# Performance work log

Measured on AMD Instinct MI355X. Metric: run time of the kernel, lower is better.

## Reference

```python
import jax, jax.numpy as jnp
import numpy as np

N_NODES = 100000
N_EDGES = 3200000
IN_DIM = 128
HID = 64


def _gcn_conv(x, src, dst, norm, W, b, n_nodes):
    # x: [N, Fin]; PyG GCNConv: h = x @ W^T, propagate with sym norm, + bias
    h = x @ W.T                                  # [N, Fout]
    msg = h[src] * norm[:, None]                 # gather + scale, [E', Fout]
    out = jax.ops.segment_sum(msg, dst, num_segments=n_nodes)  # scatter-add
    return out + b


def _build_norm(edge_index, n_nodes):
    # add self-loops, compute D^-1/2 A D^-1/2 edge weights
    loops = jnp.arange(n_nodes, dtype=edge_index.dtype)
    src = jnp.concatenate([edge_index[0], loops])
    dst = jnp.concatenate([edge_index[1], loops])
    deg = jax.ops.segment_sum(jnp.ones_like(dst, dtype=jnp.float32), dst,
                              num_segments=n_nodes)
    dinv = jnp.where(deg > 0, jax.lax.rsqrt(jnp.maximum(deg, 1.0)), 0.0)
    norm = dinv[src] * dinv[dst]
    return src, dst, norm


def setup_inputs() -> dict:
    key = jax.random.key(0)
    k = jax.random.split(key, 8)
    x = jax.random.normal(k[0], (N_NODES, IN_DIM), dtype=jnp.float32)
    edge_index = jax.random.randint(k[1], (2, N_EDGES), 0, N_NODES, dtype=jnp.int64)
    s1 = 1.0 / np.sqrt(IN_DIM)
    s2 = 1.0 / np.sqrt(HID)
    W1 = jax.random.uniform(k[2], (HID, IN_DIM), jnp.float32, -s1, s1)
    b1 = jnp.zeros((HID,), jnp.float32)
    W2 = jax.random.uniform(k[3], (HID, HID), jnp.float32, -s2, s2)
    b2 = jnp.zeros((HID,), jnp.float32)
    Wc = jax.random.uniform(k[4], (1, HID), jnp.float32, -s2, s2)
    bc = jax.random.uniform(k[5], (1,), jnp.float32, -s2, s2)
    return {"x": x, "edge_index": edge_index, "W1": W1, "b1": b1,
            "W2": W2, "b2": b2, "Wc": Wc, "bc": bc}


def reference(x, edge_index, W1, b1, W2, b2, Wc, bc):
    n = x.shape[0]
    src, dst, norm = _build_norm(edge_index, n)
    h = _gcn_conv(x, src, dst, norm, W1, b1, n)
    h = jax.nn.relu(h)
    h = _gcn_conv(h, src, dst, norm, W2, b2, n)
    return h @ Wc.T + bc                          # [N, 1]
```

## Files before the change

kernel.cpp:

```cpp
#include <hip/hip_runtime.h>
#include <hip/hip_bf16.h>
#include <hip/hip_fp16.h>

#define N_NODES 100000
#define N_EDGES 3200000
#define F_IN    128
#define F_H     64

#define NBUCK 256
#define NPB   391
#define SRC_BITS 17
#define BCAP  16384
#define CAP   80

__global__ __launch_bounds__(256) void k_init(const float* __restrict__ W2,
                                              const float* __restrict__ Wc,
                                              const float* __restrict__ b2,
                                              const float* __restrict__ bc,
                                              float* __restrict__ wc2,
                                              float* __restrict__ c0,
                                              int* __restrict__ bcur) {
    int t = threadIdx.x;
    bcur[t] = t * BCAP;
    if (t < 64) {
        float s = 0.0f;
#pragma unroll 8
        for (int f = 0; f < F_H; f++) s += Wc[f] * W2[f * F_H + t];
        wc2[t] = s;
        float p = Wc[t] * b2[t];
#pragma unroll
        for (int off = 32; off > 0; off >>= 1) p += __shfl_xor(p, off, 64);
        if (t == 0) c0[0] = p + bc[0];
    }
}

#define PA_T   256
#define PA_C   4096
#define PA_PER (PA_C / PA_T)
__global__ __launch_bounds__(PA_T) void k_partA(const int* __restrict__ src,
                                                const int* __restrict__ dst,
                                                int* __restrict__ bucket_cursor,
                                                int* __restrict__ packT) {
    __shared__ int lcount[NBUCK];
    __shared__ int lstart[NBUCK];
    __shared__ int loffs[NBUCK];
    __shared__ int lbase[NBUCK];
    __shared__ int s_pack[PA_C];
    __shared__ unsigned char s_bkt[PA_C];
    __shared__ int ltot;
    int t = threadIdx.x;
    long long e0 = (long long)blockIdx.x * PA_C;
    if (t < NBUCK) lcount[t] = 0;
    __syncthreads();
    int ep[PA_PER];
    short eb[PA_PER];
#pragma unroll
    for (int i = 0; i < PA_PER; i++) {
        long long e = e0 + i * PA_T + t;
        if (e < N_EDGES) {
            int es = src[e], ed = dst[e];
            int b = ed / NPB;
            eb[i] = (short)b;
            ep[i] = ((ed - b * NPB) << SRC_BITS) | es;
            atomicAdd(&lcount[b], 1);
        } else eb[i] = -1;
    }
    __syncthreads();
    if (t < 64) {
        int base = t * 4;
        int c0 = lcount[base], c1 = lcount[base + 1], c2 = lcount[base + 2], c3 = lcount[base + 3];
        int ssum = c0 + c1 + c2 + c3;
        int sc = ssum;
#pragma unroll
        for (int off = 1; off < 64; off <<= 1) {
            int v = __shfl_up(sc, off, 64);
            if (t >= off) sc += v;
        }
        int ex = sc - ssum;
        lstart[base]     = ex;
        lstart[base + 1] = ex + c0;
        lstart[base + 2] = ex + c0 + c1;
        lstart[base + 3] = ex + c0 + c1 + c2;
        if (t == 63) ltot = sc;
    }
    __syncthreads();
    if (t < NBUCK) {
        loffs[t] = lstart[t];
        int c = lcount[t];
        lbase[t] = c ? atomicAdd(&bucket_cursor[t], c) : 0;
    }
    __syncthreads();
#pragma unroll
    for (int i = 0; i < PA_PER; i++) {
        if (eb[i] >= 0) {
            int idx = atomicAdd(&loffs[eb[i]], 1);
            s_pack[idx] = ep[i];
            s_bkt[idx] = (unsigned char)eb[i];
        }
    }
    __syncthreads();
    int tot = ltot;
    for (int i = t; i < tot; i += PA_T) {
        int b = s_bkt[i];
        int addr = lbase[b] + (i - lstart[b]);
        packT[addr] = s_pack[i];
    }
}

#define PB_T   1024
__global__ __launch_bounds__(PB_T) void k_partB(const int* __restrict__ bcur,
                                                const int* __restrict__ packT,
                                                int* __restrict__ deg,
                                                int* __restrict__ srcs) {
    __shared__ int lcnt[NPB];
    int b = blockIdx.x;
    int node0 = b * NPB;
    int nloc = min(NPB, N_NODES - node0);
    int base = b * BCAP;
    int len = bcur[b] - base;
    if (len > BCAP) len = BCAP;
    int t = threadIdx.x;
    const int SMASK = (1 << SRC_BITS) - 1;

    for (int i = t; i < NPB; i += PB_T) lcnt[i] = 0;
    __syncthreads();
    for (int i = t; i < len; i += PB_T) {
        int pk = packT[base + i];
        int dl = pk >> SRC_BITS;
        int pos = atomicAdd(&lcnt[dl], 1);
        if (pos < CAP)
            srcs[(size_t)(node0 + dl) * CAP + pos] = pk & SMASK;
    }
    __syncthreads();
    for (int i = t; i < nloc; i += PB_T) deg[node0 + i] = lcnt[i];
}

#define GT   256
#define NTB  128
#define KTT  32
#define XS   132
#define WS   68

__global__ __launch_bounds__(GT, 3) void k_gemm1(const float* __restrict__ x,
                                                 const float* __restrict__ W1,
                                                 const int* __restrict__ deg,
                                                 __half* __restrict__ hs) {
    __shared__ float xT[2][KTT * XS];
    __shared__ float wT[2][KTT * WS];
    int t = threadIdx.x;
    int wv = t >> 6, lane = t & 63;
    int h  = wv >> 1;
    int nw = wv & 1;
    int fg = lane & 7;
    int ng = lane >> 3;
    int node0 = blockIdx.x * NTB;
    int t2 = t & 127;

    float acc[8][8];
#pragma unroll
    for (int c = 0; c < 8; c++)
#pragma unroll
        for (int j = 0; j < 8; j++) acc[c][j] = 0.0f;

    for (int i = 0; i < 2; i++) {
        int k0 = h * 64 + i * KTT;
        __syncthreads();
        {
            int node = node0 + t2;
            float4 v[8];
            if (node < N_NODES) {
                const float4* xp = (const float4*)&x[(size_t)node * F_IN + k0];
#pragma unroll
                for (int j = 0; j < 8; j++) v[j] = xp[j];
            } else {
#pragma unroll
                for (int j = 0; j < 8; j++) v[j] = make_float4(0.f, 0.f, 0.f, 0.f);
            }
#pragma unroll
            for (int j = 0; j < 8; j++) {
                xT[h][(4 * j + 0) * XS + t2] = v[j].x;
                xT[h][(4 * j + 1) * XS + t2] = v[j].y;
                xT[h][(4 * j + 2) * XS + t2] = v[j].z;
                xT[h][(4 * j + 3) * XS + t2] = v[j].w;
            }
        }
        {
            int f = t2 & 63, kh = t2 >> 6;
            const float4* wp = (const float4*)&W1[(size_t)f * F_IN + k0 + kh * 16];
#pragma unroll
            for (int j = 0; j < 4; j++) {
                float4 v = wp[j];
                int kl = kh * 16 + 4 * j;
                wT[h][(kl + 0) * WS + f] = v.x;
                wT[h][(kl + 1) * WS + f] = v.y;
                wT[h][(kl + 2) * WS + f] = v.z;
                wT[h][(kl + 3) * WS + f] = v.w;
            }
        }
        __syncthreads();
#pragma unroll 4
        for (int k = 0; k < KTT; k++) {
            float4 wa = *(const float4*)&wT[h][k * WS + 8 * fg];
            float4 wb = *(const float4*)&wT[h][k * WS + 8 * fg + 4];
            float4 xa = *(const float4*)&xT[h][k * XS + nw * 64 + 8 * ng];
            float4 xb = *(const float4*)&xT[h][k * XS + nw * 64 + 8 * ng + 4];
            float wr[8] = {wa.x, wa.y, wa.z, wa.w, wb.x, wb.y, wb.z, wb.w};
            float xv[8] = {xa.x, xa.y, xa.z, xa.w, xb.x, xb.y, xb.z, xb.w};
#pragma unroll
            for (int c = 0; c < 8; c++)
#pragma unroll
                for (int j = 0; j < 8; j++) acc[c][j] += xv[c] * wr[j];
        }
    }
    float* cb = (float*)xT;
    int rb = (nw * 64 + lane) * 66;
    __syncthreads();
    if (h == 1) {
#pragma unroll
        for (int c = 0; c < 8; c++)
#pragma unroll
            for (int jj = 0; jj < 4; jj++)
                *(float2*)&cb[rb + c * 8 + 2 * jj] =
                    make_float2(acc[c][2 * jj], acc[c][2 * jj + 1]);
    }
    __syncthreads();
    if (h == 0) {
#pragma unroll
        for (int c = 0; c < 8; c++) {
            int node = node0 + nw * 64 + ng * 8 + c;
            if (node < N_NODES) {
                float dv = rsqrtf((float)(deg[node] + 1));
                float s[8];
#pragma unroll
                for (int jj = 0; jj < 4; jj++) {
                    float2 p = *(const float2*)&cb[rb + c * 8 + 2 * jj];
                    s[2 * jj]     = dv * (acc[c][2 * jj] + p.x);
                    s[2 * jj + 1] = dv * (acc[c][2 * jj + 1] + p.y);
                }
                __half2* hp = (__half2*)&hs[(size_t)node * F_H + 8 * fg];
                hp[0] = __floats2half2_rn(s[0], s[1]);
                hp[1] = __floats2half2_rn(s[2], s[3]);
                hp[2] = __floats2half2_rn(s[4], s[5]);
                hp[3] = __floats2half2_rn(s[6], s[7]);
            }
        }
    }
}

__global__ void k_agg1q(const int* __restrict__ deg, const int* __restrict__ srcs,
                        const __half* __restrict__ hs,
                        const float* __restrict__ b1, const float* __restrict__ wc2,
                        float* __restrict__ q) {
    unsigned tid = blockIdx.x * blockDim.x + threadIdx.x;
    unsigned node = tid >> 6;
    int lane = tid & 63;
    if (node >= N_NODES) return;
    int up = lane >> 5;
    int fp = lane & 31;
    const __half2* hs2 = (const __half2*)hs;

    int d = deg[node];
    int beg = (int)node * CAP;
    int end = beg + d;
    float2 acc = make_float2(0.0f, 0.0f);
    if (up == 0) {
        float2 s = __half22float2(hs2[(size_t)node * 32 + fp]);
        acc.x = s.x; acc.y = s.y;
    }
    int j = beg;
    for (; j + 16 <= end; j += 16) {
        int s[16];
#pragma unroll
        for (int u = 0; u < 16; u++) s[u] = srcs[j + u];
#pragma unroll
        for (int u = 0; u < 8; u++) {
            int sel = up ? s[2 * u + 1] : s[2 * u];
            float2 v = __half22float2(hs2[(size_t)sel * 32 + fp]);
            acc.x += v.x; acc.y += v.y;
        }
    }
    for (; j + 2 <= end; j += 2) {
        int sel = up ? srcs[j + 1] : srcs[j];
        float2 v = __half22float2(hs2[(size_t)sel * 32 + fp]);
        acc.x += v.x; acc.y += v.y;
    }
    if (j < end && up == 0) {
        float2 v = __half22float2(hs2[(size_t)srcs[j] * 32 + fp]);
        acc.x += v.x; acc.y += v.y;
    }
    acc.x += __shfl_xor(acc.x, 32, 64);
    acc.y += __shfl_xor(acc.y, 32, 64);
    float dv = rsqrtf((float)(d + 1));
    float2 bb = *(const float2*)&b1[2 * fp];
    float2 ww = *(const float2*)&wc2[2 * fp];
    float z0 = fmaxf(fmaf(dv, acc.x, bb.x), 0.0f);
    float z1 = fmaxf(fmaf(dv, acc.y, bb.y), 0.0f);
    float p = z0 * ww.x + z1 * ww.y;
#pragma unroll
    for (int off = 16; off > 0; off >>= 1)
        p += __shfl_xor(p, off, 64);
    if (lane == 0) q[node] = dv * p;
}

__global__ void k_final(const int* __restrict__ deg, const int* __restrict__ srcs,
                        const float* __restrict__ q,
                        const float* __restrict__ c0, float* __restrict__ out) {
    int node = blockIdx.x * blockDim.x + threadIdx.x;
    if (node >= N_NODES) return;
    int d = deg[node];
    int beg = node * CAP;
    int end = beg + d;
    float acc = q[node];
    int j = beg;
    for (; j + 4 <= end; j += 4) {
        int s0 = srcs[j], s1 = srcs[j + 1], s2 = srcs[j + 2], s3 = srcs[j + 3];
        float a0 = q[s0], a1 = q[s1], a2 = q[s2], a3 = q[s3];
        acc += (a0 + a1) + (a2 + a3);
    }
    for (; j < end; j++) acc += q[srcs[j]];
    out[node] = rsqrtf((float)(d + 1)) * acc + c0[0];
}

extern "C" void kernel_launch(void* const* d_in, const int* in_sizes, int n_in,
                              void* d_out, int out_size, void* d_ws, size_t ws_size,
                              hipStream_t stream) {
    const float* x  = (const float*)d_in[0];
    const int*   ei = (const int*)d_in[1];
    const int*   src = ei;
    const int*   dst = ei + N_EDGES;
    const float* W1 = (const float*)d_in[2];
    const float* b1 = (const float*)d_in[3];
    const float* W2 = (const float*)d_in[4];
    const float* b2 = (const float*)d_in[5];
    const float* Wc = (const float*)d_in[6];
    const float* bc = (const float*)d_in[7];
    float* out = (float*)d_out;

    char* w = (char*)d_ws;
    int*    bcur    = (int*)w;    w += NBUCK * 4;
    float*  wc2     = (float*)w;  w += 64 * 4;
    float*  c0      = (float*)w;  w += 4 * 4;
    int*    deg     = (int*)w;    w += (size_t)N_NODES * 4;
    float*  q       = (float*)w;  w += (size_t)N_NODES * 4;
    int*    srcs    = (int*)w;    w += (size_t)N_NODES * CAP * 4;
    char*   shared_region = w;
    int*    packT   = (int*)shared_region;
    __half* bufA    = (__half*)shared_region;
    w += (size_t)NBUCK * BCAP * 4 + 256;

    const int TB = 256;
    const int NB_PA = (int)(((long long)N_EDGES + PA_C - 1) / PA_C);
    const int NB_G  = (N_NODES + NTB - 1) / NTB;
    const int NB_AG = ((unsigned)N_NODES * 64 + TB - 1) / TB;

    k_init <<<1, 256, 0, stream>>>(W2, Wc, b2, bc, wc2, c0, bcur);
    k_partA<<<NB_PA, PA_T, 0, stream>>>(src, dst, bcur, packT);
    k_partB<<<NBUCK, PB_T, 0, stream>>>(bcur, packT, deg, srcs);

    k_gemm1<<<NB_G, GT, 0, stream>>>(x, W1, deg, bufA);

    k_agg1q<<<NB_AG, TB, 0, stream>>>(deg, srcs, bufA, b1, wc2, q);

    k_final<<<(N_NODES + TB - 1) / TB, TB, 0, stream>>>(deg, srcs, q, c0, out);
}
```

Before: 296.3 us.

## Restructure GEMM1 tiling: drop split-K reduction, use 4x8 register tiles

Rewrites the first-layer GEMM. The old kernel split K across two wave halves and reduced the partials through shared memory; the new one has every wave cover the full K in four 32-wide chunks, with 4x8 per-thread accumulator tiles instead of 8x8. Shared memory per block shrinks and the launch bound rises to 4 blocks per SIMD, aiming to raise occupancy and remove the reduction pass. In exchange there are more sync rounds, less register reuse per LDS load, and narrower 8-byte output stores.

```diff
diff --git a/kernel.cpp b/kernel.cpp
--- a/kernel.cpp
+++ b/kernel.cpp
@@ -137,112 +137,82 @@
 
 #define GT   256
 #define NTB  128
-#define KTT  32
-#define XS   132
+#define KT2  32
 #define WS   68
 
-__global__ __launch_bounds__(GT, 3) void k_gemm1(const float* __restrict__ x,
+__global__ __launch_bounds__(GT, 4) void k_gemm1(const float* __restrict__ x,
                                                  const float* __restrict__ W1,
                                                  const int* __restrict__ deg,
                                                  __half* __restrict__ hs) {
-    __shared__ float xT[2][KTT * XS];
-    __shared__ float wT[2][KTT * WS];
+    __shared__ float wT[KT2 * WS];
+    __shared__ float xT[KT2 * NTB];
     int t = threadIdx.x;
-    int wv = t >> 6, lane = t & 63;
-    int h  = wv >> 1;
-    int nw = wv & 1;
-    int fg = lane & 7;
-    int ng = lane >> 3;
     int node0 = blockIdx.x * NTB;
-    int t2 = t & 127;
-
-    float acc[8][8];
-#pragma unroll
-    for (int c = 0; c < 8; c++)
-#pragma unroll
-        for (int j = 0; j < 8; j++) acc[c][j] = 0.0f;
-
-    for (int i = 0; i < 2; i++) {
-        int k0 = h * 64 + i * KTT;
+    int lane = t & 63, wv = t >> 6;
+    int fi = lane & 15, ni = lane >> 4;
+    int n0 = wv * 32 + ni * 8;
+
+    float acc[4][8];
+#pragma unroll
+    for (int r = 0; r < 4; r++)
+#pragma unroll
+        for (int c = 0; c < 8; c++) acc[r][c] = 0.0f;
+
+    for (int p = 0; p < 4; p++) {
+        int k0 = p * KT2;
+        if (p) __syncthreads();
+        {
+            int f = t & 63, kq = t >> 6;
+            const float4* wp = (const float4*)&W1[(size_t)f * F_IN + k0 + kq * 8];
+#pragma unroll
+            for (int j = 0; j < 2; j++) {
+                float4 v = wp[j];
+                int kl = kq * 8 + 4 * j;
+                wT[(kl + 0) * WS + f] = v.x;
+                wT[(kl + 1) * WS + f] = v.y;
+                wT[(kl + 2) * WS + f] = v.z;
+                wT[(kl + 3) * WS + f] = v.w;
+            }
+        }
+        {
+            int n = t & 127, half = t >> 7;
+            int node = node0 + n;
+#pragma unroll
+            for (int j = 0; j < 4; j++) {
+                int ku = half * 4 + j;
+                float4 v = make_float4(0.f, 0.f, 0.f, 0.f);
+                if (node < N_NODES)
+                    v = *(const float4*)&x[(size_t)node * F_IN + k0 + 4 * ku];
+                int kl = 4 * ku;
+                xT[(kl + 0) * NTB + n] = v.x;
+                xT[(kl + 1) * NTB + n] = v.y;
+                xT[(kl + 2) * NTB + n] = v.z;
+                xT[(kl + 3) * NTB + n] = v.w;
+            }
+        }
         __syncthreads();
-        {
-            int node = node0 + t2;
-            float4 v[8];
-            if (node < N_NODES) {
-                const float4* xp = (const float4*)&x[(size_t)node * F_IN + k0];
-#pragma unroll
-                for (int j = 0; j < 8; j++) v[j] = xp[j];
-            } else {
-#pragma unroll
-                for (int j = 0; j < 8; j++) v[j] = make_float4(0.f, 0.f, 0.f, 0.f);
-            }
-#pragma unroll
-            for (int j = 0; j < 8; j++) {
-                xT[h][(4 * j + 0) * XS + t2] = v[j].x;
-                xT[h][(4 * j + 1) * XS + t2] = v[j].y;
-                xT[h][(4 * j + 2) * XS + t2] = v[j].z;
-                xT[h][(4 * j + 3) * XS + t2] = v[j].w;
-            }
-        }
-        {
-            int f = t2 & 63, kh = t2 >> 6;
-            const float4* wp = (const float4*)&W1[(size_t)f * F_IN + k0 + kh * 16];
-#pragma unroll
-            for (int j = 0; j < 4; j++) {
-                float4 v = wp[j];
-                int kl = kh * 16 + 4 * j;
-                wT[h][(kl + 0) * WS + f] = v.x;
-                wT[h][(kl + 1) * WS + f] = v.y;
-                wT[h][(kl + 2) * WS + f] = v.z;
-                wT[h][(kl + 3) * WS + f] = v.w;
-            }
-        }
-        __syncthreads();
-#pragma unroll 4
-        for (int k = 0; k < KTT; k++) {
-            float4 wa = *(const float4*)&wT[h][k * WS + 8 * fg];
-            float4 wb = *(const float4*)&wT[h][k * WS + 8 * fg + 4];
-            float4 xa = *(const float4*)&xT[h][k * XS + nw * 64 + 8 * ng];
-            float4 xb = *(const float4*)&xT[h][k * XS + nw * 64 + 8 * ng + 4];
-            float wr[8] = {wa.x, wa.y, wa.z, wa.w, wb.x, wb.y, wb.z, wb.w};
+#pragma unroll 8
+        for (int k = 0; k < KT2; k++) {
+            float4 wf = *(const float4*)&wT[k * WS + fi * 4];
+            float4 xa = *(const float4*)&xT[k * NTB + n0];
+            float4 xb = *(const float4*)&xT[k * NTB + n0 + 4];
+            float wr[4] = {wf.x, wf.y, wf.z, wf.w};
             float xv[8] = {xa.x, xa.y, xa.z, xa.w, xb.x, xb.y, xb.z, xb.w};
 #pragma unroll
-            for (int c = 0; c < 8; c++)
-#pragma unroll
-                for (int j = 0; j < 8; j++) acc[c][j] += xv[c] * wr[j];
-        }
-    }
-    float* cb = (float*)xT;
-    int rb = (nw * 64 + lane) * 66;
-    __syncthreads();
-    if (h == 1) {
-#pragma unroll
-        for (int c = 0; c < 8; c++)
-#pragma unroll
-            for (int jj = 0; jj < 4; jj++)
-                *(float2*)&cb[rb + c * 8 + 2 * jj] =
-                    make_float2(acc[c][2 * jj], acc[c][2 * jj + 1]);
-    }
-    __syncthreads();
-    if (h == 0) {
-#pragma unroll
-        for (int c = 0; c < 8; c++) {
-            int node = node0 + nw * 64 + ng * 8 + c;
-            if (node < N_NODES) {
-                float dv = rsqrtf((float)(deg[node] + 1));
-                float s[8];
-#pragma unroll
-                for (int jj = 0; jj < 4; jj++) {
-                    float2 p = *(const float2*)&cb[rb + c * 8 + 2 * jj];
-                    s[2 * jj]     = dv * (acc[c][2 * jj] + p.x);
-                    s[2 * jj + 1] = dv * (acc[c][2 * jj + 1] + p.y);
-                }
-                __half2* hp = (__half2*)&hs[(size_t)node * F_H + 8 * fg];
-                hp[0] = __floats2half2_rn(s[0], s[1]);
-                hp[1] = __floats2half2_rn(s[2], s[3]);
-                hp[2] = __floats2half2_rn(s[4], s[5]);
-                hp[3] = __floats2half2_rn(s[6], s[7]);
-            }
+            for (int r = 0; r < 4; r++)
+#pragma unroll
+                for (int c = 0; c < 8; c++) acc[r][c] += wr[r] * xv[c];
+        }
+    }
+#pragma unroll
+    for (int c = 0; c < 8; c++) {
+        int node = node0 + n0 + c;
+        if (node < N_NODES) {
+            float dv = rsqrtf((float)(deg[node] + 1));
+            __half2 h0 = __floats2half2_rn(acc[0][c] * dv, acc[1][c] * dv);
+            __half2 h1 = __floats2half2_rn(acc[2][c] * dv, acc[3][c] * dv);
+            __half2* hp = (__half2*)&hs[(size_t)node * F_H + fi * 4];
+            hp[0] = h0; hp[1] = h1;
         }
     }
 }
```

New measurement: 294.9 us. No clear change (-0.4%).
